# Optimization experiments

Measured on AMD Instinct MI355X. Metric: run time of the kernel, lower is better.

The kernel has to match this reference:

```python
import jax, jax.numpy as jnp
import numpy as np

# MUCMA: multiuser CMA adaptive MIMO FIR equalizer (commplax af.mucma)
# framed_signal: (N, taps, dims) complex, carried as re/im float32 pairs.
N, TAPS, DIMS, DELTA = 131072, 19, 2, 6
LR = 2.0 ** (-13)
BETA = 0.999
R2 = 1.32  # E|a|^4 / E|a|^2 for unit-power 16QAM constellation


def setup_inputs() -> dict:
    key = jax.random.key(0)
    k1, k2 = jax.random.split(key)
    fr_re = jax.random.normal(k1, (N, TAPS, DIMS), dtype=jnp.float32) * 0.7071
    fr_im = jax.random.normal(k2, (N, TAPS, DIMS), dtype=jnp.float32) * 0.7071
    # initial MIMO weights: identity at the center tap (commplax mucma init)
    w0_re = np.zeros((DIMS, DIMS, TAPS), dtype=np.float32)
    ctap = (TAPS + 1) // 2 - 1
    w0_re[np.arange(DIMS), np.arange(DIMS), ctap] = 1.0
    return {
        'fr_re': fr_re,
        'fr_im': fr_im,
        'w0_re': jnp.asarray(w0_re),
        'w0_im': jnp.zeros((DIMS, DIMS, TAPS), jnp.float32),
    }


def _mucma_forward(fr_re, fr_im, w0_re, w0_im):
    u_all = fr_re + 1j * fr_im                      # (N, taps, dims) complex64
    w0 = (w0_re + 1j * w0_im).astype(u_all.dtype)   # (dims, dims, taps)
    # mask kills self cross-correlation terms (k == l)
    mask = (1.0 - jnp.eye(DIMS, dtype=jnp.float32))[:, :, None]

    def step(carry, u):
        # u: (taps, dims) frame of input samples
        w, z, r, bp = carry
        v = jnp.einsum('ijt,tj->i', w, u)                     # MIMO FIR output, (dims,)
        z = jnp.concatenate((v[None, :], z[:-1]))             # output delay line, (delta, dims)
        # running cross-correlation r[k,l,d] ~ E[z_k(n) z_l(n-d)^*]
        r = BETA * r + (1.0 - BETA) * jnp.einsum('k,dl->kld', v, z.conj())
        rhat = (r / (1.0 - bp)) * mask                        # bias-corrected, off-diagonal only
        e = R2 - jnp.abs(v) ** 2                              # CMA modulus error, (dims,) real
        loss = jnp.sum(e ** 2) + 2.0 * jnp.sum(jnp.abs(rhat) ** 2)
        uc = u.conj().T[None, :, :]                           # (1, dims, taps)
        g_cma = -2.0 * e[:, None, None] * v[:, None, None] * uc
        g_mu = 2.0 * jnp.einsum('kld,dl->k', rhat, z.conj())[:, None, None] * uc
        w_new = w - LR * (g_cma + g_mu)
        bp = bp * BETA
        # emit the weights USED for this symbol (pre-update), as commplax does
        return (w_new, z, r, bp), (w, loss)

    z0 = jnp.zeros((DELTA, DIMS), u_all.dtype)
    r0 = jnp.zeros((DIMS, DIMS, DELTA), u_all.dtype)
    carry0 = (w0, z0, r0, jnp.float32(BETA))
    _, (ws, _losses) = jax.lax.scan(step, carry0, u_all)
    # apply: per-symbol MIMO filtering with the recorded weight trace
    sig = jnp.einsum('nijt,ntj->ni', ws, u_all)               # (N, dims) complex
    return jnp.stack([sig.real, sig.imag], axis=-1)           # (N, dims, 2) float32


def reference(fr_re, fr_im, w0_re, w0_im):
    return _mucma_forward(fr_re, fr_im, w0_re, w0_im)
```

## Files before the change

### kernel.cpp

```cpp
#include <hip/hip_runtime.h>
#include <stdint.h>


typedef float v2f __attribute__((ext_vector_type(2)));
typedef float v4f __attribute__((ext_vector_type(4), aligned(8)));

constexpr int   NTAPS   = 19;
constexpr int   FRST    = 38;
constexpr float BETA_C  = 0.999f;
constexpr float OMB_C   = 0.001f;
constexpr float LR_C    = 0.0001220703125f;
constexpr float R2_C    = 1.32f;
constexpr int   SPLIT_N = 24576;

template <int CTRL>
__device__ __forceinline__ float dpp_add(float x) {
    return x + __int_as_float(__builtin_amdgcn_update_dpp(
        0, __float_as_int(x), CTRL, 0xF, 0xF, true));
}
template <int CTRL>
__device__ __forceinline__ float dpp_mov(float x) {
    return __int_as_float(__builtin_amdgcn_update_dpp(
        0, __float_as_int(x), CTRL, 0xF, 0xF, true));
}
__device__ __forceinline__ float rowred_bcast(float x) {
    x = dpp_add<0x121>(x);
    x = dpp_add<0x122>(x);
    x = dpp_add<0x124>(x);
    x = dpp_add<0x128>(x);
    return x;
}
__device__ __forceinline__ void plane32_swap(float& a, float& b) {
    asm("s_nop 1\n\t"
        "v_permlane32_swap_b32 %0, %1\n\t"
        "s_nop 1"
        : "+v"(a), "+v"(b));
}
__device__ __forceinline__ void plane32_swap2(float& a, float& b, float& c, float& d) {
    asm("s_nop 1\n\t"
        "v_permlane32_swap_b32 %0, %1\n\t"
        "v_permlane32_swap_b32 %2, %3\n\t"
        "s_nop 1"
        : "+v"(a), "+v"(b), "+v"(c), "+v"(d));
}
__device__ __forceinline__ void wg_barrier() {
    asm volatile("s_waitcnt lgkmcnt(0)\n\ts_barrier" ::: "memory");
}

__global__ void __launch_bounds__(64)
gram7_kernel(const float* __restrict__ fr_re, const float* __restrict__ fr_im,
             float* __restrict__ sc, int nsym)
{
    __shared__ float lre[71 * FRST], lim[71 * FRST];
    const int lane = threadIdx.x;
    const int n0   = blockIdx.x * 64;
    const int base = (n0 - 7) * FRST;
    const long gmax = (long)nsym * FRST;
    for (int idx = lane; idx < 71 * FRST; idx += 64) {
        const long g = (long)base + idx;
        float a = 0.f, b = 0.f;
        if (g >= 0 && g < gmax) { a = fr_re[g]; b = fr_im[g]; }
        lre[idx] = a; lim[idx] = b;
    }
    __syncthreads();
    const int m = n0 + lane;
    if (m >= nsym) return;
    const float* br = lre + (lane + 7) * FRST;
    const float* bi = lim + (lane + 7) * FRST;
    float out[16];
#pragma unroll
    for (int k = 1; k <= 7; ++k) {
        const float* ar = br - k * FRST;
        const float* ai = bi - k * FRST;
        float sr = 0.f, si = 0.f;
#pragma unroll
        for (int e = 0; e < FRST; ++e) {
            sr = fmaf(ar[e], br[e], fmaf(ai[e], bi[e], sr));
            si = fmaf(-ai[e], br[e], fmaf(ar[e], bi[e], si));
        }
        const bool ok = (m >= k);
        out[2*(k-1)]   = ok ? sr : 0.f;
        out[2*(k-1)+1] = ok ? si : 0.f;
    }
    out[14] = 0.f; out[15] = 0.f;
    float* d = sc + (size_t)m * 16;
#pragma unroll
    for (int j = 0; j < 4; ++j)
        *(v4f*)(d + 4*j) = (v4f){out[4*j], out[4*j+1], out[4*j+2], out[4*j+3]};
}

struct A_St {
    float acr[8], aci[8];
    float histr[8], histi[8];
    v4f   scr[4][4];
    float z_re, z_im, r_re, r_im, bp;
};
struct A_Ctx {
    const float* scp; float* outp;
    float (*aring)[2][32][2]; float (*cring)[2][32][2];
    int h, sl; bool d0f, csel; int last;
};

template <int S, bool EARLY, bool TAIL>
__device__ __forceinline__ void a_pos(A_St& st, const A_Ctx& c, int SB)
{
    constexpr int s8 = S & 7, s4 = S & 3, NC = 4 + (S & 3);
    const int m = SB + S;

    float vr = st.acr[s8], vi = st.aci[s8];
#pragma unroll
    for (int k = 1; k <= NC; ++k) {
        const float hr = st.histr[(S - k) & 7];
        const float hi = st.histi[(S - k) & 7];
        const v4f sv = st.scr[s4][(k - 1) >> 1];
        const float Sr = (k & 1) ? sv.x : sv.z;
        const float Si = (k & 1) ? sv.y : sv.w;
        vr = fmaf(-hr, Sr, fmaf( hi, Si, vr));
        vi = fmaf(-hr, Si, fmaf(-hi, Sr, vi));
    }

    *(v2f*)(c.outp + 4 * (size_t)m + 2 * c.h) = (v2f){vr, vi};

    float Xr = vr, Yr = vr, Xi = vi, Yi = vi;
    plane32_swap2(Xr, Yr, Xi, Yi);
    const float vlr = c.csel ? Xr : Yr;
    const float vli = c.csel ? Xi : Yi;

    const float zsr = dpp_mov<0x111>(st.z_re);
    const float zsi = dpp_mov<0x111>(st.z_im);
    st.z_re = c.d0f ? vlr : zsr;
    st.z_im = c.d0f ? vli : zsi;

    const float ar = OMB_C * vr, ai = OMB_C * vi;
    st.r_re = BETA_C * st.r_re + (ar * st.z_re + ai * st.z_im);
    st.r_im = BETA_C * st.r_im + (ai * st.z_re - ar * st.z_im);

    float qr = st.r_re * st.z_re + st.r_im * st.z_im;
    float qi = st.r_im * st.z_re - st.r_re * st.z_im;
    qr = rowred_bcast(qr);
    qi = rowred_bcast(qi);

    float i2;
    if (EARLY) {
        const float inv = __builtin_amdgcn_rcpf(1.0f - st.bp);
        st.bp *= BETA_C;
        i2 = (2.0f * LR_C) * inv;
    } else {
        i2 = 2.0f * LR_C;
    }
    const float t  = vr * vr + vi * vi;
    const float e2 = fmaf(2.0f * LR_C, t, -(2.0f * LR_C) * R2_C);
    const float cr = fmaf(e2, vr, i2 * qr);
    const float ci = fmaf(e2, vi, i2 * qi);

    st.histr[s8] = cr; st.histi[s8] = ci;
    *(v2f*)&c.cring[s8][c.h][c.sl][0] = (v2f){cr, ci};

    int mp = m + 4;
    if (TAIL) { if (mp > c.last) mp = c.last; }
    const float* p = c.scp + (size_t)mp * 16;
#pragma unroll
    for (int j = 0; j < 4; ++j)
        st.scr[s4][j] = *(const v4f*)(p + 4 * j);
}

template <int I, bool EARLY, bool TAIL>
__device__ __forceinline__ void a_sub(A_St& st, const A_Ctx& c, int SB)
{
#pragma unroll
    for (int t = 0; t < 4; ++t) {
        const v2f a0 = *(const v2f*)&c.aring[(4*I + t) & 7][c.h][0][0];
        st.acr[(4*I + t) & 7] = a0.x;
        st.aci[(4*I + t) & 7] = a0.y;
    }
    a_pos<4*I + 0, EARLY, TAIL>(st, c, SB);
    a_pos<4*I + 1, EARLY, TAIL>(st, c, SB);
    a_pos<4*I + 2, EARLY, TAIL>(st, c, SB);
    a_pos<4*I + 3, EARLY, TAIL>(st, c, SB);
    wg_barrier();
}
template <bool EARLY, bool TAIL>
__device__ __forceinline__ void a_super(A_St& st, const A_Ctx& c, int SB)
{
    a_sub<0, EARLY, TAIL>(st, c, SB);
    a_sub<1, EARLY, TAIL>(st, c, SB);
    a_sub<2, EARLY, TAIL>(st, c, SB);
    a_sub<3, EARLY, TAIL>(st, c, SB);
}

struct B_St {
    v2f wA_r, wA_i, wB_r, wB_i;
    v4f ur[16], ui[16];
    float mA, mB;
};
struct B_Ctx {
    const float* pre; const float* pim;
    float (*aring)[2][32][2]; float (*cring)[2][32][2];
    int h, sl; int last;
};

__device__ __forceinline__ v2f b_tree(const B_St& s, const v4f& uR, const v4f& uI) {
    const v2f uA_r = {uR.x,uR.y}, uB_r = {uR.z,uR.w};
    const v2f uA_i = {uI.x,uI.y}, uB_i = {uI.z,uI.w};
    v2f tr = s.wA_r*uA_r - s.wA_i*uA_i + s.wB_r*uB_r - s.wB_i*uB_i;
    v2f ti = s.wA_r*uA_i + s.wA_i*uA_r + s.wB_r*uB_i + s.wB_i*uB_r;
    return (v2f){ rowred_bcast(tr.x + tr.y), rowred_bcast(ti.x + ti.y) };
}

template <int I, bool TAIL>
__device__ __forceinline__ void b_sub(B_St& st, const B_Ctx& c, int SB)
{
    float ccr[4], cci[4];
#pragma unroll
    for (int t = 0; t < 4; ++t) {
        const v2f cc = *(const v2f*)&c.cring[(4*I + 4 + t) & 7][c.h][0][0];
        ccr[t] = cc.x; cci[t] = cc.y;
    }
#pragma unroll
    for (int t = 0; t < 4; ++t) {
        const float crA = ccr[t] * st.mA, ciA = cci[t] * st.mA;
        const float crB = ccr[t] * st.mB, ciB = cci[t] * st.mB;
        const v4f uR = st.ur[(4*I + 12 + t) & 15], uI = st.ui[(4*I + 12 + t) & 15];
        const v2f uA_r = {uR.x,uR.y}, uB_r = {uR.z,uR.w};
        const v2f uA_i = {uI.x,uI.y}, uB_i = {uI.z,uI.w};
        st.wA_r -= (v2f){crA,crA}*uA_r + (v2f){ciA,ciA}*uA_i;
        st.wA_i -= (v2f){ciA,ciA}*uA_r - (v2f){crA,crA}*uA_i;
        st.wB_r -= (v2f){crB,crB}*uB_r + (v2f){ciB,ciB}*uB_i;
        st.wB_i -= (v2f){ciB,ciB}*uB_r - (v2f){crB,crB}*uB_i;
    }
#pragma unroll
    for (int t = 0; t < 4; ++t) {
        const v2f T = b_tree(st, st.ur[(4*I + 4 + t) & 15], st.ui[(4*I + 4 + t) & 15]);
        *(v2f*)&c.aring[(4*I + 4 + t) & 7][c.h][c.sl][0] = T;
    }
#pragma unroll
    for (int t = 0; t < 4; ++t) {
        int f = SB + 4*I + 8 + t;
        if (TAIL) { if (f > c.last) f = c.last; }
        st.ur[(4*I + 8 + t) & 15] = *(const v4f*)(c.pre + (size_t)f * FRST);
        st.ui[(4*I + 8 + t) & 15] = *(const v4f*)(c.pim + (size_t)f * FRST);
    }
    wg_barrier();
}
template <bool TAIL>
__device__ __forceinline__ void b_super(B_St& st, const B_Ctx& c, int SB)
{
    b_sub<0, TAIL>(st, c, SB);
    b_sub<1, TAIL>(st, c, SB);
    b_sub<2, TAIL>(st, c, SB);
    b_sub<3, TAIL>(st, c, SB);
}

__global__ void __launch_bounds__(128, 1)
mucma2b_kernel(const float* __restrict__ fr_re, const float* __restrict__ fr_im,
               const float* __restrict__ w0r_in, const float* __restrict__ w0i_in,
               const float* __restrict__ scp, float* __restrict__ outp, int nsym)
{
    __shared__ __align__(16) float cring[8][2][32][2];
    __shared__ __align__(16) float aring[8][2][32][2];

    const int  tid  = threadIdx.x;
    const int  wid  = tid >> 6;
    const int  lane = tid & 63;
    const int  sl   = lane & 31;
    const int  h    = lane >> 5;
    const int  loff = (4*sl < 34) ? 4*sl : 34;
    const int  last = nsym - 1;
    const int  SBend = nsym - 16;

    bool csel;
    { const float own = h ? 11.f : 7.f; float v = own, X = own;
      plane32_swap(X, v); csel = (X != own); }

    if (wid == 0) {
        A_St st; A_Ctx c;
        c.scp = scp; c.outp = outp; c.aring = aring; c.cring = cring;
        c.h = h; c.sl = sl; c.d0f = ((sl & 15) == 10); c.csel = csel; c.last = last;
#pragma unroll
        for (int k = 0; k < 8; ++k) {
            st.histr[k] = 0.f; st.histi[k] = 0.f;
            st.acr[k] = 0.f;  st.aci[k] = 0.f;
        }
        st.z_re = 0.f; st.z_im = 0.f; st.r_re = 0.f; st.r_im = 0.f; st.bp = BETA_C;
#pragma unroll
        for (int s = 0; s < 4; ++s)
#pragma unroll
            for (int j = 0; j < 4; ++j)
                st.scr[s][j] = *(const v4f*)(scp + (size_t)s * 16 + 4 * j);
        if (lane < 32) cring[lane >> 2][(lane >> 1) & 1][0][lane & 1] = 0.f;
        wg_barrier();

        int SB = 0;
        for (; SB < SPLIT_N; SB += 16) a_super<true , false>(st, c, SB);
        for (; SB < SBend;   SB += 16) a_super<false, false>(st, c, SB);
        a_super<false, true>(st, c, SB);
    } else {
        B_St st; B_Ctx c;
        c.pre = fr_re + loff; c.pim = fr_im + loff;
        c.aring = aring; c.cring = cring; c.h = h; c.sl = sl; c.last = last;
        st.mA = (sl <= 8) ? 1.f : 0.f;
        st.mB = (sl <= 9) ? 1.f : 0.f;
        st.wA_r = (v2f){0.f,0.f}; st.wA_i = (v2f){0.f,0.f};
        st.wB_r = (v2f){0.f,0.f}; st.wB_i = (v2f){0.f,0.f};
        if (sl <= 8) {
            const int b = h*FRST + 2*sl;
            st.wA_r.x = w0r_in[b];       st.wA_r.y = w0r_in[b+NTAPS];
            st.wA_i.x = w0i_in[b];       st.wA_i.y = w0i_in[b+NTAPS];
            st.wB_r.x = w0r_in[b+1];     st.wB_r.y = w0r_in[b+NTAPS+1];
            st.wB_i.x = w0i_in[b+1];     st.wB_i.y = w0i_in[b+NTAPS+1];
        } else if (sl == 9) {
            st.wB_r.x = w0r_in[h*FRST+18];  st.wB_r.y = w0r_in[h*FRST+37];
            st.wB_i.x = w0i_in[h*FRST+18];  st.wB_i.y = w0i_in[h*FRST+37];
        }
#pragma unroll
        for (int k = 0; k < 12; ++k) {
            st.ur[k] = *(const v4f*)(c.pre + (size_t)k * FRST);
            st.ui[k] = *(const v4f*)(c.pim + (size_t)k * FRST);
        }
#pragma unroll
        for (int k = 12; k < 16; ++k) {
            st.ur[k] = (v4f){0.f,0.f,0.f,0.f};
            st.ui[k] = (v4f){0.f,0.f,0.f,0.f};
        }
#pragma unroll
        for (int t = 0; t < 4; ++t) {
            const v2f T = b_tree(st, st.ur[t], st.ui[t]);
            *(v2f*)&aring[t][h][sl][0] = T;
        }
        wg_barrier();

        int SB = 0;
        for (; SB < SBend; SB += 16) b_super<false>(st, c, SB);
        b_super<true>(st, c, SB);
    }
}

__global__ void __launch_bounds__(64, 1)
mucma_scan_fb(const float* __restrict__ fr_re, const float* __restrict__ fr_im,
              const float* __restrict__ w0r_in, const float* __restrict__ w0i_in,
              float* __restrict__ out, int nsym)
{
    const int  lane = threadIdx.x;
    const int  sl   = lane & 31;
    const int  h    = lane >> 5;
    const int  loff = (4 * sl < 34) ? 4 * sl : 34;
    const float mA  = (sl <= 8) ? 1.f : 0.f;
    const float mB  = (sl <= 9) ? 1.f : 0.f;
    const bool d0f  = (sl == 10);
    const bool stfl = (sl == 0);

    v2f wA_r = {0.f,0.f}, wA_i = {0.f,0.f}, wB_r = {0.f,0.f}, wB_i = {0.f,0.f};
    if (sl <= 8) {
        const int b = h * FRST + 2 * sl;
        wA_r.x = w0r_in[b];         wA_r.y = w0r_in[b + NTAPS];
        wA_i.x = w0i_in[b];         wA_i.y = w0i_in[b + NTAPS];
        wB_r.x = w0r_in[b + 1];     wB_r.y = w0r_in[b + NTAPS + 1];
        wB_i.x = w0i_in[b + 1];     wB_i.y = w0i_in[b + NTAPS + 1];
    } else if (sl == 9) {
        wB_r.x = w0r_in[h * FRST + 18];  wB_r.y = w0r_in[h * FRST + 37];
        wB_i.x = w0i_in[h * FRST + 18];  wB_i.y = w0i_in[h * FRST + 37];
    }
    float r_re = 0.f, r_im = 0.f, z_re = 0.f, z_im = 0.f;
    float bp = BETA_C;

    bool csel;
    {
        const float own = h ? 11.f : 7.f;
        float v = own, X = own;
        plane32_swap(X, v);
        csel = (X != own);
    }

    const float* pre = fr_re + loff;
    const float* pim = fr_im + loff;

    v4f rr[8], ri[8];
#pragma unroll
    for (int p = 0; p < 8; ++p) {
        const int idx = (p < nsym) ? p : (nsym - 1);
        rr[p] = *(const v4f*)(pre + (size_t)idx * FRST);
        ri[p] = *(const v4f*)(pim + (size_t)idx * FRST);
    }

    auto body = [&](int n, int p, int npf) {
        const v4f uR = rr[p], uI = ri[p];
        rr[p] = *(const v4f*)(pre + (size_t)npf * FRST);
        ri[p] = *(const v4f*)(pim + (size_t)npf * FRST);

        const v2f uA_r = {uR.x, uR.y}, uB_r = {uR.z, uR.w};
        const v2f uA_i = {uI.x, uI.y}, uB_i = {uI.z, uI.w};

        v2f tr = wA_r * uA_r - wA_i * uA_i + wB_r * uB_r - wB_i * uB_i;
        v2f ti = wA_r * uA_i + wA_i * uA_r + wB_r * uB_i + wB_i * uB_r;
        float xr = rowred_bcast(tr.x + tr.y);
        float xi = rowred_bcast(ti.x + ti.y);
        const float vkr = xr, vki = xi;

        float Xr = xr, Xi = xi;
        plane32_swap(Xr, xr);
        plane32_swap(Xi, xi);
        const float vlr = csel ? Xr : xr;
        const float vli = csel ? Xi : xi;

        const float zsr = dpp_mov<0x111>(z_re);
        const float zsi = dpp_mov<0x111>(z_im);
        z_re = d0f ? vlr : zsr;
        z_im = d0f ? vli : zsi;

        const float ar = OMB_C * vkr, ai = OMB_C * vki;
        r_re = BETA_C * r_re + (ar * z_re + ai * z_im);
        r_im = BETA_C * r_im + (ai * z_re - ar * z_im);

        float qr = r_re * z_re + r_im * z_im;
        float qi = r_im * z_re - r_re * z_im;
        qr = rowred_bcast(qr);
        qi = rowred_bcast(qi);

        const float inv = __builtin_amdgcn_rcpf(1.0f - bp);
        bp *= BETA_C;
        const float i2 = (2.0f * LR_C) * inv;
        const float ek = R2_C - (vkr * vkr + vki * vki);
        const float e2 = (-2.0f * LR_C) * ek;
        const float cr = e2 * vkr + i2 * qr;
        const float ci = e2 * vki + i2 * qi;

        const float crA = cr * mA, ciA = ci * mA;
        const float crB = cr * mB, ciB = ci * mB;
        wA_r -= (v2f){crA,crA} * uA_r + (v2f){ciA,ciA} * uA_i;
        wA_i -= (v2f){ciA,ciA} * uA_r - (v2f){crA,crA} * uA_i;
        wB_r -= (v2f){crB,crB} * uB_r + (v2f){ciB,ciB} * uB_i;
        wB_i -= (v2f){ciB,ciB} * uB_r - (v2f){crB,crB} * uB_i;

        if (stfl) {
            v2f o; o.x = vkr; o.y = vki;
            *(v2f*)(out + 4 * (size_t)n + 2 * h) = o;
        }
    };

    int NBmain = nsym / 8 - 1;
    if (NBmain < 0) NBmain = 0;
    for (int b = 0; b < NBmain; ++b) {
        const int nb = b * 8;
#pragma unroll
        for (int p = 0; p < 8; ++p) body(nb + p, p, nb + p + 8);
    }
    for (int nb = NBmain * 8; nb < nsym; nb += 8) {
#pragma unroll
        for (int p = 0; p < 8; ++p) {
            const int n = nb + p;
            if (n < nsym) {
                int npf = n + 8;
                if (npf > nsym - 1) npf = nsym - 1;
                body(n, p, npf);
            }
        }
    }
}

extern "C" void kernel_launch(void* const* d_in, const int* in_sizes, int n_in,
                              void* d_out, int out_size, void* d_ws, size_t ws_size,
                              hipStream_t stream)
{
    const float* fr_re = (const float*)d_in[0];
    const float* fr_im = (const float*)d_in[1];
    const float* w0r   = (const float*)d_in[2];
    const float* w0i   = (const float*)d_in[3];
    float* outp = (float*)d_out;
    const int nsym = in_sizes[0] / FRST;

    const bool use2 = (nsym % 16 == 0) && (nsym >= SPLIT_N + 16)
                   && (ws_size >= (size_t)nsym * 64);
    if (use2) {
        hipLaunchKernelGGL(gram7_kernel, dim3((nsym + 63) / 64), dim3(64), 0, stream,
                           fr_re, fr_im, (float*)d_ws, nsym);
        hipLaunchKernelGGL(mucma2b_kernel, dim3(1), dim3(128), 0, stream,
                           fr_re, fr_im, w0r, w0i, (const float*)d_ws, outp, nsym);
    } else {
        hipLaunchKernelGGL(mucma_scan_fb, dim3(1), dim3(64), 0, stream,
                           fr_re, fr_im, w0r, w0i, outp, nsym);
    }
}
```

Baseline: 27.11 ms.

## Precompute partial Gram correction off the critical path with packed math

Widens the Gram scratch layout to 28 floats per symbol, storing {sr,si,si,-sr} so complex FMAs can be done as packed v2 operations. In the serial A-wave recurrence, the contributions from older history terms are now accumulated into a partial sum for the next symbol right after the current correction is produced. Only the newest history term is left on the dependency chain. This shortens the per-symbol latency of the sequential scan, in exchange for more scratch memory traffic, more registers and extra loads of the larger records.

```diff
diff --git a/kernel.cpp b/kernel.cpp
--- a/kernel.cpp
+++ b/kernel.cpp
@@ -2,8 +2,9 @@
 #include <stdint.h>
 
 
-typedef float v2f __attribute__((ext_vector_type(2)));
-typedef float v4f __attribute__((ext_vector_type(4), aligned(8)));
+typedef float v2f  __attribute__((ext_vector_type(2)));
+typedef float v4f  __attribute__((ext_vector_type(4), aligned(8)));
+typedef float v4fa __attribute__((ext_vector_type(4), aligned(16)));
 
 constexpr int   NTAPS   = 19;
 constexpr int   FRST    = 38;
@@ -46,10 +47,15 @@
 __device__ __forceinline__ void wg_barrier() {
     asm volatile("s_waitcnt lgkmcnt(0)\n\ts_barrier" ::: "memory");
 }
+__device__ __forceinline__ v2f cfma_pk(v2f acc, v2f h, v4fa T) {
+    acc += (v2f){-h.x, -h.x} * (v2f){T.x, T.y};
+    acc += (v2f){ h.y,  h.y} * (v2f){T.z, T.w};
+    return acc;
+}
 
 __global__ void __launch_bounds__(64)
-gram7_kernel(const float* __restrict__ fr_re, const float* __restrict__ fr_im,
-             float* __restrict__ sc, int nsym)
+gram7p_kernel(const float* __restrict__ fr_re, const float* __restrict__ fr_im,
+              float* __restrict__ sc, int nsym)
 {
     __shared__ float lre[71 * FRST], lim[71 * FRST];
     const int lane = threadIdx.x;
@@ -67,7 +73,7 @@
     if (m >= nsym) return;
     const float* br = lre + (lane + 7) * FRST;
     const float* bi = lim + (lane + 7) * FRST;
-    float out[16];
+    float* d = sc + (size_t)m * 28;
 #pragma unroll
     for (int k = 1; k <= 7; ++k) {
         const float* ar = br - k * FRST;
@@ -78,22 +84,18 @@
             sr = fmaf(ar[e], br[e], fmaf(ai[e], bi[e], sr));
             si = fmaf(-ai[e], br[e], fmaf(ar[e], bi[e], si));
         }
-        const bool ok = (m >= k);
-        out[2*(k-1)]   = ok ? sr : 0.f;
-        out[2*(k-1)+1] = ok ? si : 0.f;
-    }
-    out[14] = 0.f; out[15] = 0.f;
-    float* d = sc + (size_t)m * 16;
-#pragma unroll
-    for (int j = 0; j < 4; ++j)
-        *(v4f*)(d + 4*j) = (v4f){out[4*j], out[4*j+1], out[4*j+2], out[4*j+3]};
+        if (m < k) { sr = 0.f; si = 0.f; }
+        *(v4fa*)(d + (k - 1) * 4) = (v4fa){sr, si, si, -sr};
+    }
 }
 
 struct A_St {
-    float acr[8], aci[8];
-    float histr[8], histi[8];
-    v4f   scr[4][4];
-    float z_re, z_im, r_re, r_im, bp;
+    v2f  acor2[8];
+    v2f  hist2[8];
+    v2f  ppart;
+    v4fa scr[4][7];
+    v2f  z2, r2;
+    float bp;
 };
 struct A_Ctx {
     const float* scp; float* outp;
@@ -104,41 +106,34 @@
 template <int S, bool EARLY, bool TAIL>
 __device__ __forceinline__ void a_pos(A_St& st, const A_Ctx& c, int SB)
 {
-    constexpr int s8 = S & 7, s4 = S & 3, NC = 4 + (S & 3);
+    constexpr int s8 = S & 7, s4 = S & 3, t = S & 3;
+    constexpr int SN = S + 1, s4n = SN & 3, NCn = 4 + (SN & 3);
     const int m = SB + S;
 
-    float vr = st.acr[s8], vi = st.aci[s8];
-#pragma unroll
-    for (int k = 1; k <= NC; ++k) {
-        const float hr = st.histr[(S - k) & 7];
-        const float hi = st.histi[(S - k) & 7];
-        const v4f sv = st.scr[s4][(k - 1) >> 1];
-        const float Sr = (k & 1) ? sv.x : sv.z;
-        const float Si = (k & 1) ? sv.y : sv.w;
-        vr = fmaf(-hr, Sr, fmaf( hi, Si, vr));
-        vi = fmaf(-hr, Si, fmaf(-hi, Sr, vi));
-    }
-
-    *(v2f*)(c.outp + 4 * (size_t)m + 2 * c.h) = (v2f){vr, vi};
-
-    float Xr = vr, Yr = vr, Xi = vi, Yi = vi;
+    const v2f h1 = st.hist2[(S + 7) & 7];
+    v2f v2 = st.acor2[s8] + st.ppart;
+    v2 = cfma_pk(v2, h1, st.scr[s4][0]);
+
+    *(v2f*)(c.outp + 4 * (size_t)m + 2 * c.h) = v2;
+
+    float Xr = v2.x, Yr = v2.x, Xi = v2.y, Yi = v2.y;
     plane32_swap2(Xr, Yr, Xi, Yi);
     const float vlr = c.csel ? Xr : Yr;
     const float vli = c.csel ? Xi : Yi;
 
-    const float zsr = dpp_mov<0x111>(st.z_re);
-    const float zsi = dpp_mov<0x111>(st.z_im);
-    st.z_re = c.d0f ? vlr : zsr;
-    st.z_im = c.d0f ? vli : zsi;
-
-    const float ar = OMB_C * vr, ai = OMB_C * vi;
-    st.r_re = BETA_C * st.r_re + (ar * st.z_re + ai * st.z_im);
-    st.r_im = BETA_C * st.r_im + (ai * st.z_re - ar * st.z_im);
-
-    float qr = st.r_re * st.z_re + st.r_im * st.z_im;
-    float qi = st.r_im * st.z_re - st.r_re * st.z_im;
-    qr = rowred_bcast(qr);
-    qi = rowred_bcast(qi);
+    const float zsr = dpp_mov<0x111>(st.z2.x);
+    const float zsi = dpp_mov<0x111>(st.z2.y);
+    st.z2.x = c.d0f ? vlr : zsr;
+    st.z2.y = c.d0f ? vli : zsi;
+
+    const v2f va = (v2f){OMB_C, OMB_C} * v2;
+    const v2f zx = (v2f){st.z2.x, st.z2.x};
+    const v2f zy = (v2f){st.z2.y, st.z2.y};
+    st.r2 = (v2f){BETA_C, BETA_C} * st.r2 + va * zx + (v2f){va.y, -va.x} * zy;
+
+    const v2f q2 = st.r2 * zx + (v2f){st.r2.y, -st.r2.x} * zy;
+    const float qr = rowred_bcast(q2.x);
+    const float qi = rowred_bcast(q2.y);
 
     float i2;
     if (EARLY) {
@@ -148,31 +143,37 @@
     } else {
         i2 = 2.0f * LR_C;
     }
-    const float t  = vr * vr + vi * vi;
-    const float e2 = fmaf(2.0f * LR_C, t, -(2.0f * LR_C) * R2_C);
-    const float cr = fmaf(e2, vr, i2 * qr);
-    const float ci = fmaf(e2, vi, i2 * qi);
-
-    st.histr[s8] = cr; st.histi[s8] = ci;
-    *(v2f*)&c.cring[s8][c.h][c.sl][0] = (v2f){cr, ci};
-
-    int mp = m + 4;
-    if (TAIL) { if (mp > c.last) mp = c.last; }
-    const float* p = c.scp + (size_t)mp * 16;
-#pragma unroll
-    for (int j = 0; j < 4; ++j)
-        st.scr[s4][j] = *(const v4f*)(p + 4 * j);
+    const float tt = v2.x * v2.x + v2.y * v2.y;
+    const float e2 = fmaf(2.0f * LR_C, tt, -(2.0f * LR_C) * R2_C);
+    const v2f c2 = (v2f){e2, e2} * v2 + (v2f){i2, i2} * (v2f){qr, qi};
+
+    *(v2f*)&c.cring[s8][c.h][c.sl][0] = c2;
+    st.hist2[s8] = c2;
+
+    {
+        v2f pp = {0.f, 0.f};
+#pragma unroll
+        for (int k = 2; k <= NCn; ++k)
+            pp = cfma_pk(pp, st.hist2[(SN - k) & 7], st.scr[s4n][k - 1]);
+        st.ppart = pp;
+    }
+
+    {
+        int mp = m + 4;
+        if (TAIL) { if (mp > c.last) mp = c.last; }
+        const float* p = c.scp + (size_t)mp * 28;
+#pragma unroll
+        for (int j = 0; j < 4 + t; ++j)
+            st.scr[s4][j] = *(const v4fa*)(p + 4 * j);
+    }
 }
 
 template <int I, bool EARLY, bool TAIL>
 __device__ __forceinline__ void a_sub(A_St& st, const A_Ctx& c, int SB)
 {
 #pragma unroll
-    for (int t = 0; t < 4; ++t) {
-        const v2f a0 = *(const v2f*)&c.aring[(4*I + t) & 7][c.h][0][0];
-        st.acr[(4*I + t) & 7] = a0.x;
-        st.aci[(4*I + t) & 7] = a0.y;
-    }
+    for (int t = 0; t < 4; ++t)
+        st.acor2[(4*I + t) & 7] = *(const v2f*)&c.aring[(4*I + t) & 7][c.h][0][0];
     a_pos<4*I + 0, EARLY, TAIL>(st, c, SB);
     a_pos<4*I + 1, EARLY, TAIL>(st, c, SB);
     a_pos<4*I + 2, EARLY, TAIL>(st, c, SB);
@@ -252,7 +253,7 @@
 }
 
 __global__ void __launch_bounds__(128, 1)
-mucma2b_kernel(const float* __restrict__ fr_re, const float* __restrict__ fr_im,
+mucma2c_kernel(const float* __restrict__ fr_re, const float* __restrict__ fr_im,
                const float* __restrict__ w0r_in, const float* __restrict__ w0i_in,
                const float* __restrict__ scp, float* __restrict__ outp, int nsym)
 {
@@ -278,15 +279,18 @@
         c.h = h; c.sl = sl; c.d0f = ((sl & 15) == 10); c.csel = csel; c.last = last;
 #pragma unroll
         for (int k = 0; k < 8; ++k) {
-            st.histr[k] = 0.f; st.histi[k] = 0.f;
-            st.acr[k] = 0.f;  st.aci[k] = 0.f;
-        }
-        st.z_re = 0.f; st.z_im = 0.f; st.r_re = 0.f; st.r_im = 0.f; st.bp = BETA_C;
-#pragma unroll
-        for (int s = 0; s < 4; ++s)
-#pragma unroll
-            for (int j = 0; j < 4; ++j)
-                st.scr[s][j] = *(const v4f*)(scp + (size_t)s * 16 + 4 * j);
+            st.hist2[k] = (v2f){0.f, 0.f};
+            st.acor2[k] = (v2f){0.f, 0.f};
+        }
+        st.ppart = (v2f){0.f, 0.f};
+        st.z2 = (v2f){0.f, 0.f}; st.r2 = (v2f){0.f, 0.f}; st.bp = BETA_C;
+#pragma unroll
+        for (int s = 0; s < 4; ++s) {
+            const float* p = scp + s * 28;
+#pragma unroll
+            for (int j = 0; j < 4 + s; ++j)
+                st.scr[s][j] = *(const v4fa*)(p + 4 * j);
+        }
         if (lane < 32) cring[lane >> 2][(lane >> 1) & 1][0][lane & 1] = 0.f;
         wg_barrier();
 
@@ -469,11 +473,11 @@
     const int nsym = in_sizes[0] / FRST;
 
     const bool use2 = (nsym % 16 == 0) && (nsym >= SPLIT_N + 16)
-                   && (ws_size >= (size_t)nsym * 64);
+                   && (ws_size >= (size_t)nsym * 112 + 1024);
     if (use2) {
-        hipLaunchKernelGGL(gram7_kernel, dim3((nsym + 63) / 64), dim3(64), 0, stream,
+        hipLaunchKernelGGL(gram7p_kernel, dim3((nsym + 63) / 64), dim3(64), 0, stream,
                            fr_re, fr_im, (float*)d_ws, nsym);
-        hipLaunchKernelGGL(mucma2b_kernel, dim3(1), dim3(128), 0, stream,
+        hipLaunchKernelGGL(mucma2c_kernel, dim3(1), dim3(128), 0, stream,
                            fr_re, fr_im, w0r, w0i, (const float*)d_ws, outp, nsym);
     } else {
         hipLaunchKernelGGL(mucma_scan_fb, dim3(1), dim3(64), 0, stream,
```

New measurement: 36.94 ms. 36.2% more time.
